# Optimization experiments

Hardware: AMD Instinct MI355X
Metric: run time of the kernel (lower is better)

The kernel has to match this reference:

```python
import jax, jax.numpy as jnp
import numpy as np

B, S, DIN, DOUT = 4, 2048, 4096, 16384


def setup_inputs() -> dict:
    key = jax.random.key(0)
    k1, k2, k3, k4 = jax.random.split(key, 4)
    hidden_states = jax.random.normal(k1, (B, S, DIN), dtype=jnp.float32)
    # int8-valued quantized weight, per-output-channel symmetric quantization
    w_int8 = jax.random.randint(k2, (DOUT, DIN), -127, 128, dtype=jnp.int32)
    # per-output-channel dequant scale (small positive)
    w_scale = jax.random.uniform(k3, (DOUT,), dtype=jnp.float32, minval=1e-4, maxval=2e-2)
    bias = jax.random.normal(k4, (DOUT,), dtype=jnp.float32)
    return {"hidden_states": hidden_states, "w_int8": w_int8,
            "w_scale": w_scale, "bias": bias}


def reference(hidden_states, w_int8, w_scale, bias):
    # Q8Linear with fuse_gelu=True: dequantized int8 matmul + bias + GELU.
    # Dequant is folded as (x @ W_q^T) * scale_o (per output channel).
    acc = jnp.einsum('bsd,od->bso', hidden_states,
                     w_int8.astype(jnp.float32))          # [B,S,DOUT]
    y = acc * w_scale + bias                               # per-channel dequant + bias
    # fused GELU (kernel uses tanh approximation)
    return jax.nn.gelu(y, approximate=True)
```

## Files before the change

### kernel.cpp

```cpp
#include <hip/hip_runtime.h>
#include <math.h>

#define M_DIM 8192
#define N_DIM 16384
#define K_DIM 4096
#define KTILES (K_DIM / 64)

typedef _Float16 half8 __attribute__((ext_vector_type(8)));
typedef _Float16 half4v __attribute__((ext_vector_type(4)));
typedef float f32x4 __attribute__((ext_vector_type(4)));
typedef int i32x4 __attribute__((ext_vector_type(4)));

#define GLOAD_LDS16(gp, lp)                                                     \
  __builtin_amdgcn_global_load_lds(                                             \
      (const __attribute__((address_space(1))) unsigned int*)(gp),              \
      (__attribute__((address_space(3))) unsigned int*)(lp), 16, 0, 0)

__device__ __forceinline__ float gelu_tanh(float y) {
  float t = tanhf(0.7978845608028654f * (y + 0.044715f * y * y * y));
  return 0.5f * y * (1.0f + t);
}

__global__ void cvt_f32_to_f16_k(const float* __restrict__ in,
                                 _Float16* __restrict__ out, int n8) {
  int i = blockIdx.x * blockDim.x + threadIdx.x;
  if (i >= n8) return;
  const f32x4* p = (const f32x4*)in + 2 * (size_t)i;
  f32x4 a = __builtin_nontemporal_load(p);
  f32x4 b = __builtin_nontemporal_load(p + 1);
  half8 h;
  h[0] = (_Float16)a[0]; h[1] = (_Float16)a[1];
  h[2] = (_Float16)a[2]; h[3] = (_Float16)a[3];
  h[4] = (_Float16)b[0]; h[5] = (_Float16)b[1];
  h[6] = (_Float16)b[2]; h[7] = (_Float16)b[3];
  ((half8*)out)[i] = h;
}

__global__ void cvt_i32_to_f16_k(const int* __restrict__ in,
                                 _Float16* __restrict__ out, int n8) {
  int i = blockIdx.x * blockDim.x + threadIdx.x;
  if (i >= n8) return;
  const i32x4* p = (const i32x4*)in + 2 * (size_t)i;
  i32x4 a = __builtin_nontemporal_load(p);
  i32x4 b = __builtin_nontemporal_load(p + 1);
  half8 h;
  h[0] = (_Float16)(float)a[0]; h[1] = (_Float16)(float)a[1];
  h[2] = (_Float16)(float)a[2]; h[3] = (_Float16)(float)a[3];
  h[4] = (_Float16)(float)b[0]; h[5] = (_Float16)(float)b[1];
  h[6] = (_Float16)(float)b[2]; h[7] = (_Float16)(float)b[3];
  ((half8*)out)[i] = h;
}

__global__ __launch_bounds__(512, 2) void q8gemm_gelu_256(
    const _Float16* __restrict__ Ah, const _Float16* __restrict__ Wh,
    const float* __restrict__ w_scale, const float* __restrict__ bias,
    float* __restrict__ out) {
  __shared__ _Float16 sA[2][256 * 64];
  __shared__ _Float16 sB[2][256 * 64];

  const int tid = threadIdx.x;
  const int lane = tid & 63;
  const int wave = tid >> 6;
  const int ln15 = lane & 15;
  const int quad = lane >> 4;
  const int waveM = wave >> 2;
  const int waveN = wave & 3;

  int bid = blockIdx.x;
  int swz = (bid & 7) * 256 + (bid >> 3);
  int group = swz >> 9;
  int within = swz & 511;
  int pid_m = (group << 3) + (within & 7);
  int pid_n = within >> 3;

  const int rowA0 = pid_m * 256;
  const int rowB0 = pid_n * 256;

  const int srow = wave * 8 + (lane >> 3);
  const int kswz = ((lane & 7) ^ ((lane >> 3) & 7)) << 3;
  const _Float16* gA = Ah + (size_t)(rowA0 + srow) * K_DIM + kswz;
  const _Float16* gB = Wh + (size_t)(rowB0 + srow) * K_DIM + kswz;
  const int ldst = wave * 512;

  const int swzb = (ln15 & 7) << 4;
  const int kq = quad << 4;
  const int aK0 = ((kq ^ swzb) >> 1);
  const int aK1 = (((64 | kq) ^ swzb) >> 1);
  const int aRowBase = (waveM * 128 + ln15) * 64;
  const int bRowBase = (waveN * 64 + ln15) * 64;

  f32x4 acc[8][4] = {};

#pragma unroll
  for (int i = 0; i < 4; i++) {
    GLOAD_LDS16(gA + (size_t)i * 64 * K_DIM, &sA[0][i * 4096 + ldst]);
    GLOAD_LDS16(gB + (size_t)i * 64 * K_DIM, &sB[0][i * 4096 + ldst]);
  }
  __syncthreads();

#pragma unroll 2
  for (int t = 0; t < KTILES; ++t) {
    const int cur = t & 1;
    if (t + 1 < KTILES) {
      const _Float16* ga = gA + (size_t)(t + 1) * 64;
      const _Float16* gb = gB + (size_t)(t + 1) * 64;
#pragma unroll
      for (int i = 0; i < 4; i++) {
        GLOAD_LDS16(ga + (size_t)i * 64 * K_DIM, &sA[cur ^ 1][i * 4096 + ldst]);
        GLOAD_LDS16(gb + (size_t)i * 64 * K_DIM, &sB[cur ^ 1][i * 4096 + ldst]);
      }
    }
    const _Float16* As = sA[cur];
    const _Float16* Bs = sB[cur];

    half8 af[4][2], bf[4][2];

#pragma unroll
    for (int n = 0; n < 2; n++) {
      bf[n][0] = *(const half8*)&Bs[bRowBase + n * 1024 + aK0];
      bf[n][1] = *(const half8*)&Bs[bRowBase + n * 1024 + aK1];
    }
#pragma unroll
    for (int m = 0; m < 4; m++) {
      af[m][0] = *(const half8*)&As[aRowBase + m * 1024 + aK0];
      af[m][1] = *(const half8*)&As[aRowBase + m * 1024 + aK1];
    }
    __builtin_amdgcn_s_barrier();
    __builtin_amdgcn_s_setprio(1);
#pragma unroll
    for (int m = 0; m < 4; m++)
#pragma unroll
      for (int n = 0; n < 2; n++) {
        acc[m][n] = __builtin_amdgcn_mfma_f32_16x16x32_f16(af[m][0], bf[n][0],
                                                           acc[m][n], 0, 0, 0);
        acc[m][n] = __builtin_amdgcn_mfma_f32_16x16x32_f16(af[m][1], bf[n][1],
                                                           acc[m][n], 0, 0, 0);
      }
    __builtin_amdgcn_s_setprio(0);
    __builtin_amdgcn_s_barrier();

#pragma unroll
    for (int n = 2; n < 4; n++) {
      bf[n][0] = *(const half8*)&Bs[bRowBase + n * 1024 + aK0];
      bf[n][1] = *(const half8*)&Bs[bRowBase + n * 1024 + aK1];
    }
    __builtin_amdgcn_s_barrier();
    __builtin_amdgcn_s_setprio(1);
#pragma unroll
    for (int m = 0; m < 4; m++)
#pragma unroll
      for (int n = 2; n < 4; n++) {
        acc[m][n] = __builtin_amdgcn_mfma_f32_16x16x32_f16(af[m][0], bf[n][0],
                                                           acc[m][n], 0, 0, 0);
        acc[m][n] = __builtin_amdgcn_mfma_f32_16x16x32_f16(af[m][1], bf[n][1],
                                                           acc[m][n], 0, 0, 0);
      }
    __builtin_amdgcn_s_setprio(0);
    __builtin_amdgcn_s_barrier();

#pragma unroll
    for (int m = 0; m < 4; m++) {
      af[m][0] = *(const half8*)&As[aRowBase + (m + 4) * 1024 + aK0];
      af[m][1] = *(const half8*)&As[aRowBase + (m + 4) * 1024 + aK1];
    }
    __builtin_amdgcn_s_barrier();
    __builtin_amdgcn_s_setprio(1);
#pragma unroll
    for (int m = 0; m < 4; m++)
#pragma unroll
      for (int n = 2; n < 4; n++) {
        acc[m + 4][n] = __builtin_amdgcn_mfma_f32_16x16x32_f16(
            af[m][0], bf[n][0], acc[m + 4][n], 0, 0, 0);
        acc[m + 4][n] = __builtin_amdgcn_mfma_f32_16x16x32_f16(
            af[m][1], bf[n][1], acc[m + 4][n], 0, 0, 0);
      }
    __builtin_amdgcn_s_setprio(0);
    __builtin_amdgcn_s_barrier();

    __builtin_amdgcn_s_setprio(1);
#pragma unroll
    for (int m = 0; m < 4; m++)
#pragma unroll
      for (int n = 0; n < 2; n++) {
        acc[m + 4][n] = __builtin_amdgcn_mfma_f32_16x16x32_f16(
            af[m][0], bf[n][0], acc[m + 4][n], 0, 0, 0);
        acc[m + 4][n] = __builtin_amdgcn_mfma_f32_16x16x32_f16(
            af[m][1], bf[n][1], acc[m + 4][n], 0, 0, 0);
      }
    __builtin_amdgcn_s_setprio(0);

    __syncthreads();
  }

#pragma unroll
  for (int n = 0; n < 4; n++) {
    int col = rowB0 + waveN * 64 + n * 16 + ln15;
    float sc = w_scale[col];
    float bi = bias[col];
#pragma unroll
    for (int m = 0; m < 8; m++) {
      int r0 = rowA0 + waveM * 128 + m * 16 + quad * 4;
#pragma unroll
      for (int r = 0; r < 4; r++) {
        float y = acc[m][n][r] * sc + bi;
        __builtin_nontemporal_store(gelu_tanh(y),
                                    &out[(size_t)(r0 + r) * N_DIM + col]);
      }
    }
  }
}

__global__ void q8gemm_gelu_fb(const float* __restrict__ Af,
                               const int* __restrict__ Wi,
                               const float* __restrict__ w_scale,
                               const float* __restrict__ bias,
                               float* __restrict__ out) {
  __shared__ _Float16 sA[128 * 32];
  __shared__ _Float16 sB[128 * 32];

  const int tid = threadIdx.x;
  const int lane = tid & 63;
  const int wave = tid >> 6;
  const int ln15 = lane & 15;
  const int quad = lane >> 4;
  const int waveM = wave >> 1;
  const int waveN = wave & 1;

  int bid = blockIdx.x;
  int group_id = bid >> 10;
  int within = bid & 1023;
  int pid_m = group_id * 8 + (within & 7);
  int pid_n = within >> 3;

  const int rowA0 = pid_m * 128;
  const int rowB0 = pid_n * 128;

  f32x4 acc[4][4] = {};

  int aOff[4], bOff[4];
#pragma unroll
  for (int i = 0; i < 4; i++) {
    aOff[i] = (waveM * 64 + i * 16 + ln15) * 32 + quad * 8;
    bOff[i] = (waveN * 64 + i * 16 + ln15) * 32 + quad * 8;
  }

  for (int k0 = 0; k0 < K_DIM; k0 += 32) {
#pragma unroll
    for (int i = 0; i < 4; i++) {
      int c = tid + i * 256;
      int r = c >> 3;
      int col = (c & 7) << 2;
      f32x4 av = *(const f32x4*)(Af + (size_t)(rowA0 + r) * K_DIM + k0 + col);
      half4v ah;
      ah[0] = (_Float16)av[0]; ah[1] = (_Float16)av[1];
      ah[2] = (_Float16)av[2]; ah[3] = (_Float16)av[3];
      *(half4v*)&sA[r * 32 + col] = ah;
      i32x4 wv = *(const i32x4*)(Wi + (size_t)(rowB0 + r) * K_DIM + k0 + col);
      half4v wh;
      wh[0] = (_Float16)(float)wv[0]; wh[1] = (_Float16)(float)wv[1];
      wh[2] = (_Float16)(float)wv[2]; wh[3] = (_Float16)(float)wv[3];
      *(half4v*)&sB[r * 32 + col] = wh;
    }
    __syncthreads();

    half8 aF[4], bF[4];
#pragma unroll
    for (int i = 0; i < 4; i++) {
      aF[i] = *(const half8*)&sA[aOff[i]];
      bF[i] = *(const half8*)&sB[bOff[i]];
    }
#pragma unroll
    for (int mi = 0; mi < 4; mi++)
#pragma unroll
      for (int ni = 0; ni < 4; ni++)
        acc[mi][ni] = __builtin_amdgcn_mfma_f32_16x16x32_f16(
            aF[mi], bF[ni], acc[mi][ni], 0, 0, 0);

    __syncthreads();
  }

#pragma unroll
  for (int ni = 0; ni < 4; ni++) {
    int n_g = rowB0 + waveN * 64 + ni * 16 + ln15;
    float sc = w_scale[n_g];
    float bi = bias[n_g];
#pragma unroll
    for (int mi = 0; mi < 4; mi++) {
      int r0 = rowA0 + waveM * 64 + mi * 16 + quad * 4;
#pragma unroll
      for (int r = 0; r < 4; r++) {
        float y = acc[mi][ni][r] * sc + bi;
        out[(size_t)(r0 + r) * N_DIM + n_g] = gelu_tanh(y);
      }
    }
  }
}

extern "C" void kernel_launch(void* const* d_in, const int* in_sizes, int n_in,
                              void* d_out, int out_size, void* d_ws,
                              size_t ws_size, hipStream_t stream) {
  const float* hs = (const float*)d_in[0];
  const int* w8 = (const int*)d_in[1];
  const float* wsc = (const float*)d_in[2];
  const float* bs = (const float*)d_in[3];
  float* out = (float*)d_out;

  const size_t needA = (size_t)M_DIM * K_DIM * sizeof(_Float16);
  const size_t needW = (size_t)N_DIM * K_DIM * sizeof(_Float16);

  if (ws_size >= needA + needW) {
    _Float16* Ah = (_Float16*)d_ws;
    _Float16* Wh = (_Float16*)((char*)d_ws + needA);
    int n8a = M_DIM * K_DIM / 8;
    int n8w = N_DIM * K_DIM / 8;
    cvt_f32_to_f16_k<<<n8a / 256, 256, 0, stream>>>(hs, Ah, n8a);
    cvt_i32_to_f16_k<<<n8w / 256, 256, 0, stream>>>(w8, Wh, n8w);
    const int nblocks = (M_DIM / 256) * (N_DIM / 256);
    q8gemm_gelu_256<<<nblocks, 512, 0, stream>>>(Ah, Wh, wsc, bs, out);
  } else {
    const int nblocks = (M_DIM / 128) * (N_DIM / 128);
    q8gemm_gelu_fb<<<nblocks, 256, 0, stream>>>(hs, w8, wsc, bs, out);
  }
}
```

Measured before the change: 1.754 ms.

## Split K-tile into two half-stages with interleaved prefetch and partial vmcnt waits

Restructures the main GEMM loop so each 64-wide K tile is stored as two 32-wide sub-tiles with a new XOR swizzle. Global-to-LDS prefetches for the next tile are spread across the four MFMA phases rather than issued all at once at loop start. The full __syncthreads is replaced with s_waitcnt vmcnt(4) plus barrier, so in-flight loads can overlap compute. The goal is to hide memory latency and smooth the issue of loads against MFMA work, at the cost of tricky hand-counted vmcnt synchronisation that could race if the counts are wrong.

```diff
diff --git a/kernel.cpp b/kernel.cpp
--- a/kernel.cpp
+++ b/kernel.cpp
@@ -15,6 +15,8 @@
   __builtin_amdgcn_global_load_lds(                                             \
       (const __attribute__((address_space(1))) unsigned int*)(gp),              \
       (__attribute__((address_space(3))) unsigned int*)(lp), 16, 0, 0)
+
+#define MFMA16(a, b, c) __builtin_amdgcn_mfma_f32_16x16x32_f16((a), (b), (c), 0, 0, 0)
 
 __device__ __forceinline__ float gelu_tanh(float y) {
   float t = tanhf(0.7978845608028654f * (y + 0.044715f * y * y * y));
@@ -55,8 +57,8 @@
     const _Float16* __restrict__ Ah, const _Float16* __restrict__ Wh,
     const float* __restrict__ w_scale, const float* __restrict__ bias,
     float* __restrict__ out) {
-  __shared__ _Float16 sA[2][256 * 64];
-  __shared__ _Float16 sB[2][256 * 64];
+  __shared__ _Float16 sA[2][2][8192];
+  __shared__ _Float16 sB[2][2][8192];
 
   const int tid = threadIdx.x;
   const int lane = tid & 63;
@@ -76,120 +78,119 @@
   const int rowA0 = pid_m * 256;
   const int rowB0 = pid_n * 256;
 
-  const int srow = wave * 8 + (lane >> 3);
-  const int kswz = ((lane & 7) ^ ((lane >> 3) & 7)) << 3;
-  const _Float16* gA = Ah + (size_t)(rowA0 + srow) * K_DIM + kswz;
-  const _Float16* gB = Wh + (size_t)(rowB0 + srow) * K_DIM + kswz;
+  const int kx = (((lane & 3) ^ ((lane >> 3) & 3)) << 3);
+  const _Float16* pA = Ah + (size_t)(rowA0 + wave * 16 + (lane >> 2)) * K_DIM + kx;
+  const _Float16* pB = Wh + (size_t)(rowB0 + wave * 16 + (lane >> 2)) * K_DIM + kx;
   const int ldst = wave * 512;
 
-  const int swzb = (ln15 & 7) << 4;
+  const int rowA = waveM * 128 + ln15;
+  const int rowB = waveN * 64 + ln15;
   const int kq = quad << 4;
-  const int aK0 = ((kq ^ swzb) >> 1);
-  const int aK1 = (((64 | kq) ^ swzb) >> 1);
-  const int aRowBase = (waveM * 128 + ln15) * 64;
-  const int bRowBase = (waveN * 64 + ln15) * 64;
+  const int aBase = rowA * 32 + ((kq ^ (((rowA >> 1) & 3) << 4)) >> 1);
+  const int bBase = rowB * 32 + ((kq ^ (((rowB >> 1) & 3) << 4)) >> 1);
 
   f32x4 acc[8][4] = {};
 
 #pragma unroll
-  for (int i = 0; i < 4; i++) {
-    GLOAD_LDS16(gA + (size_t)i * 64 * K_DIM, &sA[0][i * 4096 + ldst]);
-    GLOAD_LDS16(gB + (size_t)i * 64 * K_DIM, &sB[0][i * 4096 + ldst]);
-  }
-  __syncthreads();
+  for (int s = 0; s < 2; s++) {
+    const _Float16* gA = pA + s * 32;
+    const _Float16* gB = pB + s * 32;
+    GLOAD_LDS16(gA, &sA[0][s][ldst]);
+    GLOAD_LDS16(gA + (size_t)128 * K_DIM, &sA[0][s][4096 + ldst]);
+    GLOAD_LDS16(gB, &sB[0][s][ldst]);
+    GLOAD_LDS16(gB + (size_t)128 * K_DIM, &sB[0][s][4096 + ldst]);
+  }
+  asm volatile("s_waitcnt vmcnt(4)\ns_barrier" ::: "memory");
 
 #pragma unroll 2
   for (int t = 0; t < KTILES; ++t) {
     const int cur = t & 1;
-    if (t + 1 < KTILES) {
-      const _Float16* ga = gA + (size_t)(t + 1) * 64;
-      const _Float16* gb = gB + (size_t)(t + 1) * 64;
-#pragma unroll
-      for (int i = 0; i < 4; i++) {
-        GLOAD_LDS16(ga + (size_t)i * 64 * K_DIM, &sA[cur ^ 1][i * 4096 + ldst]);
-        GLOAD_LDS16(gb + (size_t)i * 64 * K_DIM, &sB[cur ^ 1][i * 4096 + ldst]);
-      }
-    }
-    const _Float16* As = sA[cur];
-    const _Float16* Bs = sB[cur];
-
-    half8 af[4][2], bf[4][2];
-
-#pragma unroll
-    for (int n = 0; n < 2; n++) {
-      bf[n][0] = *(const half8*)&Bs[bRowBase + n * 1024 + aK0];
-      bf[n][1] = *(const half8*)&Bs[bRowBase + n * 1024 + aK1];
-    }
-#pragma unroll
-    for (int m = 0; m < 4; m++) {
-      af[m][0] = *(const half8*)&As[aRowBase + m * 1024 + aK0];
-      af[m][1] = *(const half8*)&As[aRowBase + m * 1024 + aK1];
+    const int nxt = cur ^ 1;
+    const _Float16* As0 = &sA[cur][0][0];
+    const _Float16* As1 = &sA[cur][1][0];
+    const _Float16* Bs0 = &sB[cur][0][0];
+    const _Float16* Bs1 = &sB[cur][1][0];
+    const bool pf = (t + 1 < KTILES);
+    const int tn = (t + 1) * 64;
+
+    half8 af[8], bf[4];
+
+#pragma unroll
+    for (int m = 0; m < 8; m++) af[m] = *(const half8*)&As0[aBase + m * 512];
+    bf[0] = *(const half8*)&Bs0[bBase];
+    bf[1] = *(const half8*)&Bs0[bBase + 512];
+    if (pf) {
+      const _Float16* g = pA + tn;
+      GLOAD_LDS16(g, &sA[nxt][0][ldst]);
+      GLOAD_LDS16(g + (size_t)128 * K_DIM, &sA[nxt][0][4096 + ldst]);
     }
     __builtin_amdgcn_s_barrier();
     __builtin_amdgcn_s_setprio(1);
 #pragma unroll
-    for (int m = 0; m < 4; m++)
-#pragma unroll
-      for (int n = 0; n < 2; n++) {
-        acc[m][n] = __builtin_amdgcn_mfma_f32_16x16x32_f16(af[m][0], bf[n][0],
-                                                           acc[m][n], 0, 0, 0);
-        acc[m][n] = __builtin_amdgcn_mfma_f32_16x16x32_f16(af[m][1], bf[n][1],
-                                                           acc[m][n], 0, 0, 0);
-      }
+    for (int m = 0; m < 8; m++) {
+      acc[m][0] = MFMA16(af[m], bf[0], acc[m][0]);
+      acc[m][1] = MFMA16(af[m], bf[1], acc[m][1]);
+    }
     __builtin_amdgcn_s_setprio(0);
     __builtin_amdgcn_s_barrier();
 
-#pragma unroll
-    for (int n = 2; n < 4; n++) {
-      bf[n][0] = *(const half8*)&Bs[bRowBase + n * 1024 + aK0];
-      bf[n][1] = *(const half8*)&Bs[bRowBase + n * 1024 + aK1];
+    bf[2] = *(const half8*)&Bs0[bBase + 1024];
+    bf[3] = *(const half8*)&Bs0[bBase + 1536];
+    if (pf) {
+      const _Float16* g = pB + tn;
+      GLOAD_LDS16(g, &sB[nxt][0][ldst]);
+      GLOAD_LDS16(g + (size_t)128 * K_DIM, &sB[nxt][0][4096 + ldst]);
     }
     __builtin_amdgcn_s_barrier();
     __builtin_amdgcn_s_setprio(1);
 #pragma unroll
-    for (int m = 0; m < 4; m++)
-#pragma unroll
-      for (int n = 2; n < 4; n++) {
-        acc[m][n] = __builtin_amdgcn_mfma_f32_16x16x32_f16(af[m][0], bf[n][0],
-                                                           acc[m][n], 0, 0, 0);
-        acc[m][n] = __builtin_amdgcn_mfma_f32_16x16x32_f16(af[m][1], bf[n][1],
-                                                           acc[m][n], 0, 0, 0);
-      }
+    for (int m = 0; m < 8; m++) {
+      acc[m][2] = MFMA16(af[m], bf[2], acc[m][2]);
+      acc[m][3] = MFMA16(af[m], bf[3], acc[m][3]);
+    }
     __builtin_amdgcn_s_setprio(0);
-    __builtin_amdgcn_s_barrier();
-
-#pragma unroll
-    for (int m = 0; m < 4; m++) {
-      af[m][0] = *(const half8*)&As[aRowBase + (m + 4) * 1024 + aK0];
-      af[m][1] = *(const half8*)&As[aRowBase + (m + 4) * 1024 + aK1];
+
+    if (pf)
+      asm volatile("s_waitcnt vmcnt(4)\ns_barrier" ::: "memory");
+    else
+      asm volatile("s_waitcnt vmcnt(0)\ns_barrier" ::: "memory");
+
+#pragma unroll
+    for (int m = 0; m < 8; m++) af[m] = *(const half8*)&As1[aBase + m * 512];
+    bf[0] = *(const half8*)&Bs1[bBase];
+    bf[1] = *(const half8*)&Bs1[bBase + 512];
+    if (pf) {
+      const _Float16* g = pA + tn + 32;
+      GLOAD_LDS16(g, &sA[nxt][1][ldst]);
+      GLOAD_LDS16(g + (size_t)128 * K_DIM, &sA[nxt][1][4096 + ldst]);
     }
     __builtin_amdgcn_s_barrier();
     __builtin_amdgcn_s_setprio(1);
 #pragma unroll
-    for (int m = 0; m < 4; m++)
-#pragma unroll
-      for (int n = 2; n < 4; n++) {
-        acc[m + 4][n] = __builtin_amdgcn_mfma_f32_16x16x32_f16(
-            af[m][0], bf[n][0], acc[m + 4][n], 0, 0, 0);
-        acc[m + 4][n] = __builtin_amdgcn_mfma_f32_16x16x32_f16(
-            af[m][1], bf[n][1], acc[m + 4][n], 0, 0, 0);
-      }
+    for (int m = 0; m < 8; m++) {
+      acc[m][0] = MFMA16(af[m], bf[0], acc[m][0]);
+      acc[m][1] = MFMA16(af[m], bf[1], acc[m][1]);
+    }
     __builtin_amdgcn_s_setprio(0);
     __builtin_amdgcn_s_barrier();
 
+    bf[2] = *(const half8*)&Bs1[bBase + 1024];
+    bf[3] = *(const half8*)&Bs1[bBase + 1536];
+    if (pf) {
+      const _Float16* g = pB + tn + 32;
+      GLOAD_LDS16(g, &sB[nxt][1][ldst]);
+      GLOAD_LDS16(g + (size_t)128 * K_DIM, &sB[nxt][1][4096 + ldst]);
+    }
+    __builtin_amdgcn_s_barrier();
     __builtin_amdgcn_s_setprio(1);
 #pragma unroll
-    for (int m = 0; m < 4; m++)
-#pragma unroll
-      for (int n = 0; n < 2; n++) {
-        acc[m + 4][n] = __builtin_amdgcn_mfma_f32_16x16x32_f16(
-            af[m][0], bf[n][0], acc[m + 4][n], 0, 0, 0);
-        acc[m + 4][n] = __builtin_amdgcn_mfma_f32_16x16x32_f16(
-            af[m][1], bf[n][1], acc[m + 4][n], 0, 0, 0);
-      }
+    for (int m = 0; m < 8; m++) {
+      acc[m][2] = MFMA16(af[m], bf[2], acc[m][2]);
+      acc[m][3] = MFMA16(af[m], bf[3], acc[m][3]);
+    }
     __builtin_amdgcn_s_setprio(0);
 
-    __syncthreads();
+    asm volatile("s_waitcnt vmcnt(4)\ns_barrier" ::: "memory");
   }
 
 #pragma unroll
@@ -220,9 +221,9 @@
 
   const int tid = threadIdx.x;
   const int lane = tid & 63;
-  const int wave = tid >> 6;
   const int ln15 = lane & 15;
   const int quad = lane >> 4;
+  const int wave = tid >> 6;
   const int waveM = wave >> 1;
   const int waveN = wave & 1;
 
@@ -273,8 +274,7 @@
     for (int mi = 0; mi < 4; mi++)
 #pragma unroll
       for (int ni = 0; ni < 4; ni++)
-        acc[mi][ni] = __builtin_amdgcn_mfma_f32_16x16x32_f16(
-            aF[mi], bF[ni], acc[mi][ni], 0, 0, 0);
+        acc[mi][ni] = MFMA16(aF[mi], bF[ni], acc[mi][ni]);
 
     __syncthreads();
   }
```

New measurement: 1.815 ms. 3.5% more time.
